# Kernel optimization log

Measured on AMD Instinct MI355X. Metric: run time of the kernel, lower is better.

Reference implementation:

```python
import jax, jax.numpy as jnp
import numpy as np

INPUT_SIZE = 3072
CORE_SIZE = 1024
OUTPUT_SIZE = 100
BATCH = 8192


def _ri(key, shape, lo, hi):
    # small-range int8 values (torch rand*scale cast to int8)
    return jax.random.randint(key, shape, lo, hi, dtype=jnp.int32).astype(jnp.int8)


def setup_inputs() -> dict:
    key = jax.random.key(0)
    ks = jax.random.split(key, 14)
    return {
        # learned int8 weights (nonzero after EQI.apply updates)
        "W_itoc": _ri(ks[0], (INPUT_SIZE, CORE_SIZE), -3, 4),
        "W_itoc_b": _ri(ks[1], (CORE_SIZE,), -3, 4),
        "W_ctoc": _ri(ks[2], (CORE_SIZE, CORE_SIZE), -3, 4),
        "W_ctoc_b": _ri(ks[3], (CORE_SIZE,), -3, 4),
        "W_ctoo": _ri(ks[4], (CORE_SIZE, OUTPUT_SIZE), -3, 4),
        "W_ctoo_b": _ri(ks[5], (OUTPUT_SIZE,), -3, 4),
        # epsilon perturbations: EPSILON_SCALE=2 -> values in {-1,0,1}
        "e_itoc": _ri(ks[6], (INPUT_SIZE, CORE_SIZE), -2, 2),
        "e_itoc_b": _ri(ks[7], (CORE_SIZE,), -2, 2),
        "e_ctoc": _ri(ks[8], (CORE_SIZE, CORE_SIZE), -2, 2),
        "e_ctoc_b": _ri(ks[9], (CORE_SIZE,), -2, 2),
        "e_ctoo": _ri(ks[10], (CORE_SIZE, OUTPUT_SIZE), -2, 2),
        "e_ctoo_b": _ri(ks[11], (OUTPUT_SIZE,), -2, 2),
        # forward activations
        "inputs": _ri(ks[12], (BATCH, INPUT_SIZE), -4, 5),
        "hiddens": _ri(ks[13], (BATCH, CORE_SIZE), -4, 5),
    }


def _addmm_i8(x, w, b):
    # int8 addmm with wraparound semantics: accumulate in int32, cast back
    # to int8 (truncation == mod-256, matching torch int8 arithmetic).
    acc = jnp.matmul(x.astype(jnp.int32), w.astype(jnp.int32)) + b.astype(jnp.int32)
    return acc.astype(jnp.int8)


def reference(W_itoc, W_itoc_b, W_ctoc, W_ctoc_b, W_ctoo, W_ctoo_b,
              e_itoc, e_itoc_b, e_ctoc, e_ctoc_b, e_ctoo, e_ctoo_b,
              inputs, hiddens):
    # layer 1: inputs -> core (weight = W + epsilon, elementwise int8 add)
    i2c = _addmm_i8(inputs, W_itoc + e_itoc, W_itoc_b + e_itoc_b)      # [B, CORE]
    # layer 2: (hiddens + projected inputs) -> core
    h2 = _addmm_i8(hiddens + i2c, W_ctoc + e_ctoc, W_ctoc_b + e_ctoc_b)  # [B, CORE]
    # layer 3: core -> output
    out = _addmm_i8(h2, W_ctoo + e_ctoo, W_ctoo_b + e_ctoo_b)          # [B, OUT]
    return (h2, out)
```

## Files before the change

### kernel.cpp

```cpp
#include <hip/hip_runtime.h>

typedef int v4i  __attribute__((ext_vector_type(4)));
typedef int v16i __attribute__((ext_vector_type(16)));

__device__ __forceinline__ int pack4i(int a, int b, int c, int d) {
  return (a & 255) | ((b & 255) << 8) | ((c & 255) << 16) | ((d & 255) << 24);
}
__device__ __forceinline__ int badd4(int a, int b) {
  return ((a & 0x7f7f7f7f) + (b & 0x7f7f7f7f)) ^ ((a ^ b) & 0x80808080);
}

__device__ __forceinline__ void async_ld16(const void* g, void* l) {
  __builtin_amdgcn_global_load_lds(
      (const __attribute__((address_space(1))) void*)g,
      (__attribute__((address_space(3))) void*)l, 16, 0, 0);
}

__device__ void pack_tile(const int* __restrict__ W, const int* __restrict__ E,
                          char* __restrict__ Bt, int K, int N,
                          int nx, int ky, char* lin) {
  const int t = threadIdx.x;
  const int n0 = nx * 64, k0 = ky * 256;
  {
    const int kk = t >> 2, c = t & 3;
    for (int p = 0; p < 4; ++p) {
      const int k = kk + (p << 6);
      const long grow = (long)(k0 + k) * N;
      #pragma unroll
      for (int i = 0; i < 4; ++i) {
        const int nl = (c << 4) + (i << 2);
        const int ng = n0 + nl;
        int a0, a1, a2, a3;
        if (ng + 3 < N) {
          int4 wv = *(const int4*)(W + grow + ng);
          int4 ev = *(const int4*)(E + grow + ng);
          a0 = wv.x + ev.x; a1 = wv.y + ev.y; a2 = wv.z + ev.z; a3 = wv.w + ev.w;
        } else {
          a0 = (ng + 0 < N) ? W[grow + ng + 0] + E[grow + ng + 0] : 0;
          a1 = (ng + 1 < N) ? W[grow + ng + 1] + E[grow + ng + 1] : 0;
          a2 = (ng + 2 < N) ? W[grow + ng + 2] + E[grow + ng + 2] : 0;
          a3 = (ng + 3 < N) ? W[grow + ng + 3] + E[grow + ng + 3] : 0;
        }
        *(int*)(lin + k * 68 + nl) = pack4i(a0, a1, a2, a3);
      }
    }
  }
  __syncthreads();
  {
    const int n = t & 63, kq = t >> 6;
    char* dst = Bt + (long)(n0 + n) * K + k0 + (kq << 6);
    int outv[16];
    #pragma unroll
    for (int g = 0; g < 16; ++g) {
      const int k = (kq << 6) + (g << 2);
      outv[g] = pack4i(lin[(k + 0) * 68 + n], lin[(k + 1) * 68 + n],
                       lin[(k + 2) * 68 + n], lin[(k + 3) * 68 + n]);
    }
    #pragma unroll
    for (int g = 0; g < 4; ++g)
      *(int4*)(dst + (g << 4)) =
          make_int4(outv[g * 4], outv[g * 4 + 1], outv[g * 4 + 2], outv[g * 4 + 3]);
  }
}

__device__ void pack_async(const int* __restrict__ src, char* __restrict__ dst,
                           long base_ints, int iters, char* stage) {
  const int t = threadIdx.x;
  const int w = t >> 6, lane = t & 63;
  for (int it = 0; it < iters; ++it) {
    const long c0 = base_ints + (long)it * 8192;
    #pragma unroll
    for (int r = 0; r < 8; ++r) {
      const int off = (r * 4 + w) * 1024;
      const int* g = src + c0 + ((off + lane * 16) >> 2);
      async_ld16(g, stage + off);
    }
    __syncthreads();
    const char* s = stage + t * 128;
    int o[8];
    #pragma unroll
    for (int g8 = 0; g8 < 8; ++g8) {
      int4 v = *(const int4*)(s + g8 * 16);
      o[g8] = pack4i(v.x, v.y, v.z, v.w);
    }
    *(int4*)(dst + c0 + t * 32)      = make_int4(o[0], o[1], o[2], o[3]);
    *(int4*)(dst + c0 + t * 32 + 16) = make_int4(o[4], o[5], o[6], o[7]);
    __syncthreads();
  }
}

__global__ __launch_bounds__(256) void pack_all_kernel(
    const int* W1, const int* E1, char* Bt1,
    const int* W2, const int* E2, char* Bt2,
    const int* W3, const int* E3, char* Bt3,
    const int* b1, const int* eb1, int* bs1,
    const int* b2, const int* eb2, int* bs2,
    const int* b3, const int* eb3, int* bs3,
    const int* X, char* X8, const int* H, char* H8) {
  __shared__ __align__(16) char smem[32768];
  const int bid = blockIdx.x;
  if (bid < 192) {
    pack_tile(W1, E1, Bt1, 3072, 1024, bid % 16, bid / 16, smem);
  } else if (bid < 256) {
    const int l = bid - 192;
    pack_tile(W2, E2, Bt2, 1024, 1024, l % 16, l / 16, smem);
  } else if (bid < 264) {
    const int l = bid - 256;
    pack_tile(W3, E3, Bt3, 1024, 100, l & 1, l >> 1, smem);
  } else if (bid == 264) {
    const int t = threadIdx.x;
    for (int i = t; i < 1024; i += 256) {
      bs1[i] = b1[i] + eb1[i];
      bs2[i] = b2[i] + eb2[i];
    }
    for (int i = t; i < 128; i += 256)
      bs3[i] = (i < 100) ? (b3[i] + eb3[i]) : 0;
  } else if (bid < 1033) {
    pack_async(X, X8, (long)(bid - 265) * 32768, 4, smem);
  } else {
    pack_async(H, H8, (long)(bid - 1033) * 32768, 4, smem);
  }
}

template<int EPI>
__global__ __launch_bounds__(256, 4) void gemm_kernel(
    const char* __restrict__ A, const char* __restrict__ Btg,
    const int* __restrict__ bsum, const char* __restrict__ H8,
    char* __restrict__ A8out, int* __restrict__ Iout, const int K) {
  __shared__ __align__(16) char smem[30720];

  const int t = threadIdx.x;
  const int bid = blockIdx.x;
  const int mt = bid & 127, nt = bid >> 7;
  const long m0 = (long)mt << 6;
  const int n0 = nt << 7;

  const int lane = t & 63, w = t >> 6;
  const int lc = lane & 31, hg = lane >> 5;

  v16i acc[2] = {};

  const int am = t >> 2, ah = t & 3;
  const char* Arow = A + (m0 + am) * (long)K + ah * 16;
  const int aoff = am * 80 + ah * 16;
  const int bm = t >> 1, bh = t & 1;
  const char* Brow = Btg + (long)(n0 + bm) * K + bh * 32;
  const int boff = bm * 80 + bh * 32;

  const int abo = lc * 80 + hg * 16;
  const int bbo = (w * 32 + lc) * 80 + hg * 16;

  int4 ar, br0, br1;
  auto LOAD = [&](int kb) {
    ar  = *(const int4*)(Arow + kb);
    br0 = *(const int4*)(Brow + kb);
    br1 = *(const int4*)(Brow + kb + 16);
  };
  auto STORE = [&](int stage) {
    char* base = smem + stage * 15360;
    *(int4*)(base + aoff) = ar;
    *(int4*)(base + 5120 + boff)      = br0;
    *(int4*)(base + 5120 + boff + 16) = br1;
  };

  const int kiters = K >> 6;
  LOAD(0);
  STORE(0);
  __syncthreads();

  for (int kt = 0; kt < kiters; ++kt) {
    if (kt + 1 < kiters) LOAD((kt + 1) << 6);
    const char* base = smem + (kt & 1) * 15360;
    const char* Ab = base + abo;
    const char* Bb = base + 5120 + bbo;
    #pragma unroll
    for (int ks = 0; ks < 2; ++ks) {
      v4i a0 = *(const v4i*)(Ab + ks * 32);
      v4i a1 = *(const v4i*)(Ab + 32 * 80 + ks * 32);
      v4i b  = *(const v4i*)(Bb + ks * 32);
      acc[0] = __builtin_amdgcn_mfma_i32_32x32x32_i8(a0, b, acc[0], 0, 0, 0);
      acc[1] = __builtin_amdgcn_mfma_i32_32x32x32_i8(a1, b, acc[1], 0, 0, 0);
    }
    if (kt + 1 < kiters) {
      STORE((kt + 1) & 1);
      __syncthreads();
    }
  }

  const int gcl = w * 32 + lc;
  const int bs = bsum[n0 + gcl];
  if (EPI == 1) {
    #pragma unroll
    for (int tm = 0; tm < 2; ++tm) {
      #pragma unroll
      for (int r = 0; r < 16; ++r) {
        const int row = tm * 32 + (hg << 2) + (r & 3) + ((r >> 2) << 3);
        Iout[(m0 + row) * 1024 + n0 + gcl] = (int)(signed char)(acc[tm][r] + bs);
      }
    }
  } else {
    __syncthreads();
    #pragma unroll
    for (int tm = 0; tm < 2; ++tm) {
      #pragma unroll
      for (int r = 0; r < 16; ++r) {
        const int row = tm * 32 + (hg << 2) + (r & 3) + ((r >> 2) << 3);
        smem[row * 144 + gcl] = (char)(acc[tm][r] + bs);
      }
    }
    __syncthreads();
    const char* src = smem + (t >> 2) * 144 + (t & 3) * 32;
    const long gm = m0 + (t >> 2);
    const long gco = gm * 1024 + n0 + (t & 3) * 32;
    int4 s0 = *(const int4*)(src);
    int4 s1 = *(const int4*)(src + 16);
    int4 h0 = *(const int4*)(H8 + gco);
    int4 h1 = *(const int4*)(H8 + gco + 16);
    s0 = make_int4(badd4(s0.x, h0.x), badd4(s0.y, h0.y),
                   badd4(s0.z, h0.z), badd4(s0.w, h0.w));
    s1 = make_int4(badd4(s1.x, h1.x), badd4(s1.y, h1.y),
                   badd4(s1.z, h1.z), badd4(s1.w, h1.w));
    *(int4*)(A8out + gco)      = s0;
    *(int4*)(A8out + gco + 16) = s1;
  }
}

__global__ __launch_bounds__(256, 2) void gemm3_kernel(
    const int* __restrict__ h2, const char* __restrict__ Btg,
    const int* __restrict__ bsum, int* __restrict__ Iout) {
  __shared__ __align__(16) char smem[23040];
  const int t = threadIdx.x;
  const int m0 = blockIdx.x << 4;
  const int lane = t & 63, w = t >> 6;
  const int l16 = lane & 15, q = lane >> 4;
  v4i acc0 = {}, acc1 = {};

  const int am = t >> 4, ah = t & 15;
  const int* Arow = h2 + (long)(m0 + am) * 1024 + ah * 4;
  const int aoff = am * 80 + ah * 4;
  const int bm = t >> 1, bh = t & 1;
  const char* Brow = Btg + (long)bm * 1024 + bh * 32;
  const int boff = bm * 80 + bh * 32;

  const int abo  = l16 * 80 + q * 16;
  const int bbo0 = (w * 32 + l16) * 80 + q * 16;
  const int bbo1 = (w * 32 + 16 + l16) * 80 + q * 16;

  int4 ar, br0, br1;
  auto LOAD = [&](int kt) {
    const int kb = kt << 6;
    ar  = *(const int4*)(Arow + kb);
    br0 = *(const int4*)(Brow + kb);
    br1 = *(const int4*)(Brow + kb + 16);
  };
  auto STORE = [&](int stage) {
    char* base = smem + stage * 11520;
    *(int*)(base + aoff) = pack4i(ar.x, ar.y, ar.z, ar.w);
    *(int4*)(base + 1280 + boff)      = br0;
    *(int4*)(base + 1280 + boff + 16) = br1;
  };
  auto MFMA = [&](int stage) {
    const char* base = smem + stage * 11520;
    v4i a  = *(const v4i*)(base + abo);
    v4i b0 = *(const v4i*)(base + 1280 + bbo0);
    v4i b1 = *(const v4i*)(base + 1280 + bbo1);
    acc0 = __builtin_amdgcn_mfma_i32_16x16x64_i8(a, b0, acc0, 0, 0, 0);
    acc1 = __builtin_amdgcn_mfma_i32_16x16x64_i8(a, b1, acc1, 0, 0, 0);
  };

  LOAD(0); STORE(0); __syncthreads();
  for (int kt = 0; kt < 16; ++kt) {
    if (kt + 1 < 16) LOAD(kt + 1);
    MFMA(kt & 1);
    if (kt + 1 < 16) { STORE((kt + 1) & 1); __syncthreads(); }
  }

  const int c0 = w * 32 + l16;
  const int c1 = c0 + 16;
  if (c0 < 100) {
    const int b = bsum[c0];
    #pragma unroll
    for (int r = 0; r < 4; ++r)
      Iout[(long)(m0 + q * 4 + r) * 100 + c0] = (int)(signed char)(acc0[r] + b);
  }
  if (c1 < 100) {
    const int b = bsum[c1];
    #pragma unroll
    for (int r = 0; r < 4; ++r)
      Iout[(long)(m0 + q * 4 + r) * 100 + c1] = (int)(signed char)(acc1[r] + b);
  }
}

extern "C" void kernel_launch(void* const* d_in, const int* in_sizes, int n_in,
                              void* d_out, int out_size, void* d_ws, size_t ws_size,
                              hipStream_t stream) {
  (void)in_sizes; (void)n_in; (void)out_size; (void)ws_size;
  const int* W1  = (const int*)d_in[0];
  const int* b1  = (const int*)d_in[1];
  const int* W2  = (const int*)d_in[2];
  const int* b2  = (const int*)d_in[3];
  const int* W3  = (const int*)d_in[4];
  const int* b3  = (const int*)d_in[5];
  const int* E1  = (const int*)d_in[6];
  const int* eb1 = (const int*)d_in[7];
  const int* E2  = (const int*)d_in[8];
  const int* eb2 = (const int*)d_in[9];
  const int* E3  = (const int*)d_in[10];
  const int* eb3 = (const int*)d_in[11];
  const int* X   = (const int*)d_in[12];
  const int* H   = (const int*)d_in[13];
  int* out = (int*)d_out;

  char* ws  = (char*)d_ws;
  char* Bt1 = ws;
  char* Bt2 = Bt1 + 3145728;
  char* Bt3 = Bt2 + 1048576;
  int*  bs1 = (int*)(Bt3 + 131072);
  int*  bs2 = bs1 + 1024;
  int*  bs3 = bs2 + 1024;
  char* A2  = (char*)(bs3 + 128);
  char* X8  = (char*)d_out;
  char* H8  = X8 + 25165824;

  pack_all_kernel<<<dim3(1289), dim3(256), 0, stream>>>(
      W1, E1, Bt1, W2, E2, Bt2, W3, E3, Bt3,
      b1, eb1, bs1, b2, eb2, bs2, b3, eb3, bs3, X, X8, H, H8);

  gemm_kernel<0><<<dim3(1024), dim3(256), 0, stream>>>(
      X8, Bt1, bs1, H8, A2, nullptr, 3072);

  gemm_kernel<1><<<dim3(1024), dim3(256), 0, stream>>>(
      A2, Bt2, bs2, nullptr, nullptr, out, 1024);

  gemm3_kernel<<<dim3(512), dim3(256), 0, stream>>>(
      out, Bt3, bs3, out + 8388608);
}
```

Baseline: 309.4 us.

## Pipeline int32-to-int8 activation packing per wave with triple-buffered async loads

Result: no change. 306.8 us (-0.9%).

```diff
diff --git a/kernel.cpp b/kernel.cpp
--- a/kernel.cpp
+++ b/kernel.cpp
@@ -64,28 +64,26 @@
 }
 
 __device__ void pack_async(const int* __restrict__ src, char* __restrict__ dst,
-                           long base_ints, int iters, char* stage) {
-  const int t = threadIdx.x;
-  const int w = t >> 6, lane = t & 63;
-  for (int it = 0; it < iters; ++it) {
-    const long c0 = base_ints + (long)it * 8192;
-    #pragma unroll
-    for (int r = 0; r < 8; ++r) {
-      const int off = (r * 4 + w) * 1024;
-      const int* g = src + c0 + ((off + lane * 16) >> 2);
-      async_ld16(g, stage + off);
-    }
-    __syncthreads();
-    const char* s = stage + t * 128;
-    int o[8];
-    #pragma unroll
-    for (int g8 = 0; g8 < 8; ++g8) {
-      int4 v = *(const int4*)(s + g8 * 16);
-      o[g8] = pack4i(v.x, v.y, v.z, v.w);
-    }
-    *(int4*)(dst + c0 + t * 32)      = make_int4(o[0], o[1], o[2], o[3]);
-    *(int4*)(dst + c0 + t * 32 + 16) = make_int4(o[4], o[5], o[6], o[7]);
-    __syncthreads();
+                           long base, int chunks, char* wbase, int lane) {
+  auto issue = [&](int c) {
+    char* stg = wbase + (c % 3) * 4096;
+    const int* g = src + base + (long)c * 1024 + lane * 4;
+    #pragma unroll
+    for (int s = 0; s < 4; ++s)
+      async_ld16(g + s * 256, stg + s * 1024);
+  };
+  issue(0);
+  issue(1);
+  for (int c = 0; c < chunks; ++c) {
+    if (c + 2 < chunks) issue(c + 2);
+    asm volatile("s_waitcnt vmcnt(8)" ::: "memory");
+    const char* stg = wbase + (c % 3) * 4096;
+    const long ob = base + (long)c * 1024;
+    #pragma unroll
+    for (int s = 0; s < 4; ++s) {
+      int4 v = *(const int4*)(stg + s * 1024 + lane * 16);
+      *(int*)(dst + ob + s * 256 + lane * 4) = pack4i(v.x, v.y, v.z, v.w);
+    }
   }
 }
 
@@ -97,7 +95,7 @@
     const int* b2, const int* eb2, int* bs2,
     const int* b3, const int* eb3, int* bs3,
     const int* X, char* X8, const int* H, char* H8) {
-  __shared__ __align__(16) char smem[32768];
+  __shared__ __align__(16) char smem[49152];
   const int bid = blockIdx.x;
   if (bid < 192) {
     pack_tile(W1, E1, Bt1, 3072, 1024, bid % 16, bid / 16, smem);
@@ -115,10 +113,16 @@
     }
     for (int i = t; i < 128; i += 256)
       bs3[i] = (i < 100) ? (b3[i] + eb3[i]) : 0;
-  } else if (bid < 1033) {
-    pack_async(X, X8, (long)(bid - 265) * 32768, 4, smem);
+  } else if (bid < 777) {
+    const int b = bid - 265;
+    const int t = threadIdx.x, w = t >> 6, lane = t & 63;
+    pack_async(X, X8, ((long)b * 48 + w * 12) * 1024, 12,
+               smem + w * 12288, lane);
   } else {
-    pack_async(H, H8, (long)(bid - 1033) * 32768, 4, smem);
+    const int b = bid - 777;
+    const int t = threadIdx.x, w = t >> 6, lane = t & 63;
+    pack_async(H, H8, ((long)b * 32 + w * 8) * 1024, 8,
+               smem + w * 12288, lane);
   }
 }
 
@@ -322,7 +326,7 @@
   char* X8  = (char*)d_out;
   char* H8  = X8 + 25165824;
 
-  pack_all_kernel<<<dim3(1289), dim3(256), 0, stream>>>(
+  pack_all_kernel<<<dim3(1033), dim3(256), 0, stream>>>(
       W1, E1, Bt1, W2, E2, Bt2, W3, E3, Bt3,
       b1, eb1, bs1, b2, eb2, bs2, b3, eb3, bs3, X, X8, H, H8);
 
```

## Split activation narrowing into separate grid-stride copy kernel

Applied to the files above, without the earlier changes.

After: 310.1 us. No clear change (+0.2%).

```diff
diff --git a/kernel.cpp b/kernel.cpp
--- a/kernel.cpp
+++ b/kernel.cpp
@@ -8,12 +8,6 @@
 }
 __device__ __forceinline__ int badd4(int a, int b) {
   return ((a & 0x7f7f7f7f) + (b & 0x7f7f7f7f)) ^ ((a ^ b) & 0x80808080);
-}
-
-__device__ __forceinline__ void async_ld16(const void* g, void* l) {
-  __builtin_amdgcn_global_load_lds(
-      (const __attribute__((address_space(1))) void*)g,
-      (__attribute__((address_space(3))) void*)l, 16, 0, 0);
 }
 
 __device__ void pack_tile(const int* __restrict__ W, const int* __restrict__ E,
@@ -63,51 +57,24 @@
   }
 }
 
-__device__ void pack_async(const int* __restrict__ src, char* __restrict__ dst,
-                           long base_ints, int iters, char* stage) {
-  const int t = threadIdx.x;
-  const int w = t >> 6, lane = t & 63;
-  for (int it = 0; it < iters; ++it) {
-    const long c0 = base_ints + (long)it * 8192;
-    #pragma unroll
-    for (int r = 0; r < 8; ++r) {
-      const int off = (r * 4 + w) * 1024;
-      const int* g = src + c0 + ((off + lane * 16) >> 2);
-      async_ld16(g, stage + off);
-    }
-    __syncthreads();
-    const char* s = stage + t * 128;
-    int o[8];
-    #pragma unroll
-    for (int g8 = 0; g8 < 8; ++g8) {
-      int4 v = *(const int4*)(s + g8 * 16);
-      o[g8] = pack4i(v.x, v.y, v.z, v.w);
-    }
-    *(int4*)(dst + c0 + t * 32)      = make_int4(o[0], o[1], o[2], o[3]);
-    *(int4*)(dst + c0 + t * 32 + 16) = make_int4(o[4], o[5], o[6], o[7]);
-    __syncthreads();
-  }
-}
-
-__global__ __launch_bounds__(256) void pack_all_kernel(
+__global__ __launch_bounds__(256) void pack_w_kernel(
     const int* W1, const int* E1, char* Bt1,
     const int* W2, const int* E2, char* Bt2,
     const int* W3, const int* E3, char* Bt3,
     const int* b1, const int* eb1, int* bs1,
     const int* b2, const int* eb2, int* bs2,
-    const int* b3, const int* eb3, int* bs3,
-    const int* X, char* X8, const int* H, char* H8) {
-  __shared__ __align__(16) char smem[32768];
+    const int* b3, const int* eb3, int* bs3) {
+  __shared__ __align__(16) char lin[256 * 68];
   const int bid = blockIdx.x;
   if (bid < 192) {
-    pack_tile(W1, E1, Bt1, 3072, 1024, bid % 16, bid / 16, smem);
+    pack_tile(W1, E1, Bt1, 3072, 1024, bid % 16, bid / 16, lin);
   } else if (bid < 256) {
     const int l = bid - 192;
-    pack_tile(W2, E2, Bt2, 1024, 1024, l % 16, l / 16, smem);
+    pack_tile(W2, E2, Bt2, 1024, 1024, l % 16, l / 16, lin);
   } else if (bid < 264) {
     const int l = bid - 256;
-    pack_tile(W3, E3, Bt3, 1024, 100, l & 1, l >> 1, smem);
-  } else if (bid == 264) {
+    pack_tile(W3, E3, Bt3, 1024, 100, l & 1, l >> 1, lin);
+  } else {
     const int t = threadIdx.x;
     for (int i = t; i < 1024; i += 256) {
       bs1[i] = b1[i] + eb1[i];
@@ -115,10 +82,23 @@
     }
     for (int i = t; i < 128; i += 256)
       bs3[i] = (i < 100) ? (b3[i] + eb3[i]) : 0;
-  } else if (bid < 1033) {
-    pack_async(X, X8, (long)(bid - 265) * 32768, 4, smem);
-  } else {
-    pack_async(H, H8, (long)(bid - 1033) * 32768, 4, smem);
+  }
+}
+
+__global__ __launch_bounds__(256) void copy_narrow_kernel(
+    const int4* __restrict__ X4, const int4* __restrict__ H4,
+    int* __restrict__ X8, int* __restrict__ H8) {
+  const long NX = 6291456;
+  const long NT = 8388608;
+  const long stride = (long)gridDim.x * blockDim.x;
+  for (long u = (long)blockIdx.x * blockDim.x + threadIdx.x; u < NT; u += stride) {
+    if (u < NX) {
+      int4 v = X4[u];
+      X8[u] = pack4i(v.x, v.y, v.z, v.w);
+    } else {
+      int4 v = H4[u - NX];
+      H8[u - NX] = pack4i(v.x, v.y, v.z, v.w);
+    }
   }
 }
 
@@ -322,9 +302,12 @@
   char* X8  = (char*)d_out;
   char* H8  = X8 + 25165824;
 
-  pack_all_kernel<<<dim3(1289), dim3(256), 0, stream>>>(
+  pack_w_kernel<<<dim3(265), dim3(256), 0, stream>>>(
       W1, E1, Bt1, W2, E2, Bt2, W3, E3, Bt3,
-      b1, eb1, bs1, b2, eb2, bs2, b3, eb3, bs3, X, X8, H, H8);
+      b1, eb1, bs1, b2, eb2, bs2, b3, eb3, bs3);
+
+  copy_narrow_kernel<<<dim3(2048), dim3(256), 0, stream>>>(
+      (const int4*)X, (const int4*)H, (int*)X8, (int*)H8);
 
   gemm_kernel<0><<<dim3(1024), dim3(256), 0, stream>>>(
       X8, Bt1, bs1, H8, A2, nullptr, 3072);
```
